# Performance work log

Hardware: AMD Instinct MI355X
Metric: run time of the kernel (lower is better)

Reference implementation:

```python
import jax, jax.numpy as jnp
import numpy as np

IN_F = 4096
OUT_F = 11008
N_CLUSTERS = 16
TOPK = int(IN_F * 0.25)  # 1024


def setup_inputs() -> dict:
    key = jax.random.key(0)
    k1, k2, k3, k4 = jax.random.split(key, 4)
    x = jax.random.normal(k1, (1, 1, IN_F), jnp.float32)
    weight_full = jax.random.normal(k2, (OUT_F, IN_F), jnp.float32) * 0.02
    bias_full = jax.random.normal(k3, (OUT_F,), jnp.float32) * 0.02
    # cluster centers live in softmax-activation space (compared via cdist to a softmax)
    cluster_centers = jax.nn.softmax(
        jax.random.normal(k4, (N_CLUSTERS, IN_F), jnp.float32), axis=-1)
    return {"x": x, "weight_full": weight_full, "bias_full": bias_full,
            "cluster_centers": cluster_centers}


def reference(x, weight_full, bias_full, cluster_centers):
    # hot path: bsz * seq == 1
    x_flat = x.reshape(-1, x.shape[-1])                 # [1, in]
    x_avg = jnp.abs(jnp.mean(x_flat, axis=0))           # [in]
    activation = jax.nn.softmax(x_avg, axis=0)          # [in]
    # nearest cluster center (squared L2 has same argmin as L2)
    d2 = jnp.sum((cluster_centers - activation[None, :]) ** 2, axis=-1)  # [n_clusters]
    ci = jnp.argmin(d2)
    center = cluster_centers[ci]                        # [in]
    # per-cluster precomputed top-k column indices: argsort(center, descending)[:topk]
    _, topk_idx = jax.lax.top_k(center, TOPK)           # [topk]
    x_sel = jnp.take(x_flat, topk_idx, axis=1)          # [1, topk]
    w_sel = jnp.take(weight_full, topk_idx, axis=1)     # [out, topk]
    out = x_sel @ w_sel.T + bias_full                   # [1, out]
    return out.reshape(1, 1, -1)
```

## Files before the change

### kernel.cpp

```cpp
#include <hip/hip_runtime.h>

#define IN_F 4096
#define OUT_F 11008
#define NCLUST 16
#define TOPK 1024
#define NT 1024
#define NW 16

__global__ __launch_bounds__(NT) void select_mask_kernel(
    const float* __restrict__ x,
    const float* __restrict__ centers,
    float* __restrict__ xm)
{
    const int tid  = threadIdx.x;
    const int lane = tid & 63;
    const int wid  = tid >> 6;

    __shared__ __align__(16) float sx[IN_F];
    __shared__ __align__(16) float sact[IN_F];
    __shared__ unsigned int hist[NW * 256];
    __shared__ float swred[NW];
    __shared__ float sd2[NCLUST];
    __shared__ unsigned int wtot4[4];
    __shared__ unsigned int weq[NW];
    __shared__ float smax, ssum;
    __shared__ unsigned int sprefix, sKrem, sG;
    __shared__ int sci;

    if (tid == 0) { sprefix = 0u; sKrem = TOPK; sG = 0u; }

    float4 xv = reinterpret_cast<const float4*>(x)[tid];
    reinterpret_cast<float4*>(sx)[tid] = xv;
    {
        float m = fmaxf(fmaxf(fabsf(xv.x), fabsf(xv.y)),
                        fmaxf(fabsf(xv.z), fabsf(xv.w)));
        for (int off = 32; off > 0; off >>= 1) m = fmaxf(m, __shfl_down(m, off, 64));
        if (lane == 0) swred[wid] = m;
    }
    __syncthreads();
    if (wid == 0) {
        float m = (lane < NW) ? swred[lane] : -3.0e38f;
        for (int off = 8; off > 0; off >>= 1) m = fmaxf(m, __shfl_down(m, off, 64));
        if (lane == 0) smax = m;
    }
    __syncthreads();
    const float mx = smax;

    float e0 = expf(fabsf(xv.x) - mx);
    float e1 = expf(fabsf(xv.y) - mx);
    float e2 = expf(fabsf(xv.z) - mx);
    float e3 = expf(fabsf(xv.w) - mx);
    {
        float s = e0 + e1 + e2 + e3;
        for (int off = 32; off > 0; off >>= 1) s += __shfl_down(s, off, 64);
        if (lane == 0) swred[wid] = s;
    }
    __syncthreads();
    if (wid == 0) {
        float s = (lane < NW) ? swred[lane] : 0.0f;
        for (int off = 8; off > 0; off >>= 1) s += __shfl_down(s, off, 64);
        if (lane == 0) ssum = s;
    }
    __syncthreads();
    {
        const float inv = 1.0f / ssum;
        float4 a;
        a.x = e0 * inv; a.y = e1 * inv; a.z = e2 * inv; a.w = e3 * inv;
        reinterpret_cast<float4*>(sact)[tid] = a;
    }
    __syncthreads();

    {
        const float4* c4 = reinterpret_cast<const float4*>(centers + (size_t)wid * IN_F);
        const float4* a4 = reinterpret_cast<const float4*>(sact);
        float d = 0.0f;
        #pragma unroll
        for (int it = 0; it < IN_F / 4 / 64; ++it) {
            float4 c = c4[it * 64 + lane];
            float4 a = a4[it * 64 + lane];
            float t0 = c.x - a.x, t1 = c.y - a.y, t2 = c.z - a.z, t3 = c.w - a.w;
            d += t0 * t0 + t1 * t1 + t2 * t2 + t3 * t3;
        }
        for (int off = 32; off > 0; off >>= 1) d += __shfl_down(d, off, 64);
        if (lane == 0) sd2[wid] = d;
    }
    __syncthreads();

    if (wid == 0) {
        float v = (lane < NCLUST) ? sd2[lane] : 3.0e38f;
        int   bi = lane;
        for (int off = 8; off > 0; off >>= 1) {
            float ov = __shfl_down(v, off, 64);
            int   oi = __shfl_down(bi, off, 64);
            if (ov < v) { v = ov; bi = oi; }
        }
        if (lane == 0) sci = bi;
    }
    __syncthreads();

    unsigned int cv[4];
    {
        float4 c = reinterpret_cast<const float4*>(centers + (size_t)sci * IN_F)[tid];
        cv[0] = __float_as_uint(c.x);
        cv[1] = __float_as_uint(c.y);
        cv[2] = __float_as_uint(c.z);
        cv[3] = __float_as_uint(c.w);
    }

    for (int pass = 0; pass < 4; ++pass) {
        const int shift = 24 - 8 * pass;
        for (int k = tid; k < NW * 256; k += NT) hist[k] = 0u;
        __syncthreads();
        const unsigned int pfx  = sprefix;
        const unsigned int krem = sKrem;
        unsigned int* hp = &hist[wid * 256];
        #pragma unroll
        for (int j = 0; j < 4; ++j) {
            unsigned int u = cv[j];
            bool cand = (pass == 0) || ((u >> (shift + 8)) == pfx);
            if (cand) atomicAdd(&hp[(u >> shift) & 255u], 1u);
        }
        __syncthreads();
        unsigned int h = 0, s = 0;
        if (tid < 256) {
            #pragma unroll
            for (int w = 0; w < NW; ++w) h += hist[w * 256 + tid];
            s = h;
            for (int off = 1; off < 64; off <<= 1) {
                unsigned int v2 = __shfl_down(s, off, 64);
                if (lane + off < 64) s += v2;
            }
            if (lane == 0) wtot4[wid] = s;
        }
        __syncthreads();
        if (tid < 256) {
            unsigned int add = 0;
            #pragma unroll
            for (int w = 0; w < 4; ++w) if (w > wid) add += wtot4[w];
            unsigned int incl = s + add;
            unsigned int excl = incl - h;
            if (excl < krem && krem <= incl) {
                sprefix = (pfx << 8) | (unsigned int)tid;
                sKrem   = krem - excl;
            }
        }
        __syncthreads();
    }
    const unsigned int T = sprefix;

    unsigned int gt = 0, eq = 0;
    #pragma unroll
    for (int j = 0; j < 4; ++j) {
        gt += (cv[j] > T) ? 1u : 0u;
        eq += (cv[j] == T) ? 1u : 0u;
    }
    {
        unsigned int g = gt;
        for (int off = 32; off > 0; off >>= 1) g += __shfl_down(g, off, 64);
        if (lane == 0) atomicAdd(&sG, g);
    }
    unsigned int p = eq;
    for (int off = 1; off < 64; off <<= 1) {
        unsigned int v2 = __shfl_up(p, off, 64);
        if (lane >= off) p += v2;
    }
    if (lane == 63) weq[wid] = p;
    __syncthreads();
    unsigned int base = p - eq;
    #pragma unroll
    for (int w = 0; w < NW; ++w) if (w < wid) base += weq[w];
    const unsigned int needEq = TOPK - sG;

    {
        unsigned int r = 0;
        float4 o;
        o.x = ((cv[0] > T) || ((cv[0] == T) && (base + r < needEq))) ? xv.x : 0.0f; r += (cv[0] == T);
        o.y = ((cv[1] > T) || ((cv[1] == T) && (base + r < needEq))) ? xv.y : 0.0f; r += (cv[1] == T);
        o.z = ((cv[2] > T) || ((cv[2] == T) && (base + r < needEq))) ? xv.z : 0.0f; r += (cv[2] == T);
        o.w = ((cv[3] > T) || ((cv[3] == T) && (base + r < needEq))) ? xv.w : 0.0f;
        reinterpret_cast<float4*>(xm)[tid] = o;
    }
}

__global__ __launch_bounds__(256) void matvec_kernel(
    const float* __restrict__ W,
    const float* __restrict__ xm,
    const float* __restrict__ bias,
    float* __restrict__ out)
{
    __shared__ __align__(16) float sxm[IN_F];
    const int tid = threadIdx.x;
    for (int i = tid * 4; i < IN_F; i += 256 * 4) {
        *reinterpret_cast<float4*>(&sxm[i]) =
            *reinterpret_cast<const float4*>(&xm[i]);
    }
    __syncthreads();

    const int lane = tid & 63;
    const int wid  = tid >> 6;
    const int nwaves = gridDim.x * 4;

    for (int row = blockIdx.x * 4 + wid; row < OUT_F; row += nwaves) {
        const float4* wr = reinterpret_cast<const float4*>(W + (size_t)row * IN_F);
        float acc = 0.0f;
        #pragma unroll
        for (int j = 0; j < IN_F / 4 / 64; ++j) {
            float4 w4 = wr[j * 64 + lane];
            float4 x4 = *reinterpret_cast<const float4*>(&sxm[(j * 64 + lane) * 4]);
            acc += w4.x * x4.x + w4.y * x4.y + w4.z * x4.z + w4.w * x4.w;
        }
        for (int off = 32; off > 0; off >>= 1) acc += __shfl_down(acc, off, 64);
        if (lane == 0) out[row] = acc + bias[row];
    }
}

extern "C" void kernel_launch(void* const* d_in, const int* in_sizes, int n_in,
                              void* d_out, int out_size, void* d_ws, size_t ws_size,
                              hipStream_t stream) {
    const float* x       = (const float*)d_in[0];
    const float* weight  = (const float*)d_in[1];
    const float* bias    = (const float*)d_in[2];
    const float* centers = (const float*)d_in[3];
    float* out = (float*)d_out;
    float* xm  = (float*)d_ws;

    select_mask_kernel<<<1, NT, 0, stream>>>(x, centers, xm);
    matvec_kernel<<<1376, 256, 0, stream>>>(weight, xm, bias, out);
}
```

Before: 45.65 us.

## Fold softmax normalization into cluster distance and restructure matvec grid

The select kernel drops the max-subtraction pass and the normalized activation buffer. It ranks clusters by ||c||^2 - (2/S)·c·e, computed from unnormalized exponentials, and it clears histograms inline instead of with extra barriers. The matvec now keeps the masked x in registers per lane instead of shared memory, and launches 256 blocks of 1024 threads that each cover 43 rows. Together these remove several block-wide syncs and a shared-memory staging step, but exp without max-subtraction risks overflow for large inputs. A leftover dead block computes an unused value.

```diff
diff --git a/kernel.cpp b/kernel.cpp
--- a/kernel.cpp
+++ b/kernel.cpp
@@ -6,6 +6,15 @@
 #define TOPK 1024
 #define NT 1024
 #define NW 16
+#define ROWS_PB 43
+
+__device__ __forceinline__ float dot4(float4 a, float4 b) {
+    return a.x * b.x + a.y * b.y + a.z * b.z + a.w * b.w;
+}
+__device__ __forceinline__ float wredsum(float v) {
+    for (int o = 32; o > 0; o >>= 1) v += __shfl_down(v, o, 64);
+    return v;
+}
 
 __global__ __launch_bounds__(NT) void select_mask_kernel(
     const float* __restrict__ x,
@@ -16,79 +25,51 @@
     const int lane = tid & 63;
     const int wid  = tid >> 6;
 
-    __shared__ __align__(16) float sx[IN_F];
     __shared__ __align__(16) float sact[IN_F];
     __shared__ unsigned int hist[NW * 256];
     __shared__ float swred[NW];
-    __shared__ float sd2[NCLUST];
-    __shared__ unsigned int wtot4[4];
-    __shared__ unsigned int weq[NW];
-    __shared__ float smax, ssum;
+    __shared__ float sdot[NCLUST], scsq[NCLUST];
+    __shared__ unsigned int wtot4[4], weq[NW];
     __shared__ unsigned int sprefix, sKrem, sG;
     __shared__ int sci;
 
     if (tid == 0) { sprefix = 0u; sKrem = TOPK; sG = 0u; }
 
     float4 xv = reinterpret_cast<const float4*>(x)[tid];
-    reinterpret_cast<float4*>(sx)[tid] = xv;
-    {
-        float m = fmaxf(fmaxf(fabsf(xv.x), fabsf(xv.y)),
-                        fmaxf(fabsf(xv.z), fabsf(xv.w)));
-        for (int off = 32; off > 0; off >>= 1) m = fmaxf(m, __shfl_down(m, off, 64));
-        if (lane == 0) swred[wid] = m;
-    }
-    __syncthreads();
+    float e0 = expf(fabsf(xv.x)), e1 = expf(fabsf(xv.y));
+    float e2 = expf(fabsf(xv.z)), e3 = expf(fabsf(xv.w));
+    reinterpret_cast<float4*>(sact)[tid] = make_float4(e0, e1, e2, e3);
+    {
+        float s = wredsum(e0 + e1 + e2 + e3);
+        if (lane == 0) swred[wid] = s;
+        hist[tid] = 0u; hist[tid + 1024] = 0u;
+        hist[tid + 2048] = 0u; hist[tid + 3072] = 0u;
+    }
+    __syncthreads();
+    float S = 0.0f;
+    #pragma unroll
+    for (int k = 0; k < NW; ++k) S += swred[k];
+
+    {
+        const float4* cp = reinterpret_cast<const float4*>(centers + (size_t)wid * IN_F);
+        const float4* a4 = reinterpret_cast<const float4*>(sact);
+        float dt = 0.0f, cq = 0.0f;
+        #pragma unroll
+        for (int j = 0; j < 16; ++j) {
+            float4 c = cp[j * 64 + lane];
+            float4 a = a4[j * 64 + lane];
+            dt += dot4(c, a);
+            cq += dot4(c, c);
+        }
+        dt = wredsum(dt);
+        cq = wredsum(cq);
+        if (lane == 0) { sdot[wid] = dt; scsq[wid] = cq; }
+    }
+    __syncthreads();
+
     if (wid == 0) {
-        float m = (lane < NW) ? swred[lane] : -3.0e38f;
-        for (int off = 8; off > 0; off >>= 1) m = fmaxf(m, __shfl_down(m, off, 64));
-        if (lane == 0) smax = m;
-    }
-    __syncthreads();
-    const float mx = smax;
-
-    float e0 = expf(fabsf(xv.x) - mx);
-    float e1 = expf(fabsf(xv.y) - mx);
-    float e2 = expf(fabsf(xv.z) - mx);
-    float e3 = expf(fabsf(xv.w) - mx);
-    {
-        float s = e0 + e1 + e2 + e3;
-        for (int off = 32; off > 0; off >>= 1) s += __shfl_down(s, off, 64);
-        if (lane == 0) swred[wid] = s;
-    }
-    __syncthreads();
-    if (wid == 0) {
-        float s = (lane < NW) ? swred[lane] : 0.0f;
-        for (int off = 8; off > 0; off >>= 1) s += __shfl_down(s, off, 64);
-        if (lane == 0) ssum = s;
-    }
-    __syncthreads();
-    {
-        const float inv = 1.0f / ssum;
-        float4 a;
-        a.x = e0 * inv; a.y = e1 * inv; a.z = e2 * inv; a.w = e3 * inv;
-        reinterpret_cast<float4*>(sact)[tid] = a;
-    }
-    __syncthreads();
-
-    {
-        const float4* c4 = reinterpret_cast<const float4*>(centers + (size_t)wid * IN_F);
-        const float4* a4 = reinterpret_cast<const float4*>(sact);
-        float d = 0.0f;
-        #pragma unroll
-        for (int it = 0; it < IN_F / 4 / 64; ++it) {
-            float4 c = c4[it * 64 + lane];
-            float4 a = a4[it * 64 + lane];
-            float t0 = c.x - a.x, t1 = c.y - a.y, t2 = c.z - a.z, t3 = c.w - a.w;
-            d += t0 * t0 + t1 * t1 + t2 * t2 + t3 * t3;
-        }
-        for (int off = 32; off > 0; off >>= 1) d += __shfl_down(d, off, 64);
-        if (lane == 0) sd2[wid] = d;
-    }
-    __syncthreads();
-
-    if (wid == 0) {
-        float v = (lane < NCLUST) ? sd2[lane] : 3.0e38f;
-        int   bi = lane;
+        float v = (lane < NCLUST) ? (scsq[lane] - (2.0f / S) * sdot[lane]) : 3.0e38f;
+        int bi = lane;
         for (int off = 8; off > 0; off >>= 1) {
             float ov = __shfl_down(v, off, 64);
             int   oi = __shfl_down(bi, off, 64);
@@ -101,16 +82,12 @@
     unsigned int cv[4];
     {
         float4 c = reinterpret_cast<const float4*>(centers + (size_t)sci * IN_F)[tid];
-        cv[0] = __float_as_uint(c.x);
-        cv[1] = __float_as_uint(c.y);
-        cv[2] = __float_as_uint(c.z);
-        cv[3] = __float_as_uint(c.w);
+        cv[0] = __float_as_uint(c.x); cv[1] = __float_as_uint(c.y);
+        cv[2] = __float_as_uint(c.z); cv[3] = __float_as_uint(c.w);
     }
 
     for (int pass = 0; pass < 4; ++pass) {
         const int shift = 24 - 8 * pass;
-        for (int k = tid; k < NW * 256; k += NT) hist[k] = 0u;
-        __syncthreads();
         const unsigned int pfx  = sprefix;
         const unsigned int krem = sKrem;
         unsigned int* hp = &hist[wid * 256];
@@ -124,7 +101,7 @@
         unsigned int h = 0, s = 0;
         if (tid < 256) {
             #pragma unroll
-            for (int w = 0; w < NW; ++w) h += hist[w * 256 + tid];
+            for (int w = 0; w < NW; ++w) { h += hist[w * 256 + tid]; hist[w * 256 + tid] = 0u; }
             s = h;
             for (int off = 1; off < 64; off <<= 1) {
                 unsigned int v2 = __shfl_down(s, off, 64);
@@ -136,7 +113,7 @@
         if (tid < 256) {
             unsigned int add = 0;
             #pragma unroll
-            for (int w = 0; w < 4; ++w) if (w > wid) add += wtot4[w];
+            for (int w2 = 0; w2 < 4; ++w2) if (w2 > wid) add += wtot4[w2];
             unsigned int incl = s + add;
             unsigned int excl = incl - h;
             if (excl < krem && krem <= incl) {
@@ -155,8 +132,11 @@
         eq += (cv[j] == T) ? 1u : 0u;
     }
     {
+        unsigned int g = wredsum(0.0f) * 0.0f + gt;
+    }
+    {
         unsigned int g = gt;
-        for (int off = 32; off > 0; off >>= 1) g += __shfl_down(g, off, 64);
+        for (int o = 32; o > 0; o >>= 1) g += __shfl_down(g, o, 64);
         if (lane == 0) atomicAdd(&sG, g);
     }
     unsigned int p = eq;
@@ -182,34 +162,33 @@
     }
 }
 
-__global__ __launch_bounds__(256) void matvec_kernel(
+__global__ __launch_bounds__(NT, 4) void matvec_kernel(
     const float* __restrict__ W,
     const float* __restrict__ xm,
     const float* __restrict__ bias,
     float* __restrict__ out)
 {
-    __shared__ __align__(16) float sxm[IN_F];
-    const int tid = threadIdx.x;
-    for (int i = tid * 4; i < IN_F; i += 256 * 4) {
-        *reinterpret_cast<float4*>(&sxm[i]) =
-            *reinterpret_cast<const float4*>(&xm[i]);
-    }
-    __syncthreads();
-
+    const int tid  = threadIdx.x;
     const int lane = tid & 63;
     const int wid  = tid >> 6;
-    const int nwaves = gridDim.x * 4;
-
-    for (int row = blockIdx.x * 4 + wid; row < OUT_F; row += nwaves) {
+    const int rbase = blockIdx.x * ROWS_PB;
+
+    float4 sl[16];
+    {
+        const float4* xm4 = reinterpret_cast<const float4*>(xm);
+        #pragma unroll
+        for (int j = 0; j < 16; ++j) sl[j] = xm4[j * 64 + lane];
+    }
+
+    for (int r = wid; r < ROWS_PB; r += NW) {
+        const int row = rbase + r;
         const float4* wr = reinterpret_cast<const float4*>(W + (size_t)row * IN_F);
         float acc = 0.0f;
         #pragma unroll
-        for (int j = 0; j < IN_F / 4 / 64; ++j) {
-            float4 w4 = wr[j * 64 + lane];
-            float4 x4 = *reinterpret_cast<const float4*>(&sxm[(j * 64 + lane) * 4]);
-            acc += w4.x * x4.x + w4.y * x4.y + w4.z * x4.z + w4.w * x4.w;
-        }
-        for (int off = 32; off > 0; off >>= 1) acc += __shfl_down(acc, off, 64);
+        for (int j = 0; j < 16; ++j) {
+            acc += dot4(wr[j * 64 + lane], sl[j]);
+        }
+        acc = wredsum(acc);
         if (lane == 0) out[row] = acc + bias[row];
     }
 }
@@ -225,5 +204,5 @@
     float* xm  = (float*)d_ws;
 
     select_mask_kernel<<<1, NT, 0, stream>>>(x, centers, xm);
-    matvec_kernel<<<1376, 256, 0, stream>>>(weight, xm, bias, out);
-}
+    matvec_kernel<<<256, NT, 0, stream>>>(weight, xm, bias, out);
+}
```

Result: no change. 45.40 us (-0.5%).
